# Kernel tuning notes

Measured on AMD Instinct MI355X. Metric: run time of the kernel, lower is better.

The kernel has to match this reference:

```python
import jax, jax.numpy as jnp
import numpy as np

B, S, D, T, H = 4, 2048, 1024, 5, 8


def setup_inputs() -> dict:
    key = jax.random.key(0)
    ks = jax.random.split(key, 12)
    sc = 0.02  # small init scale for weights so attention logits stay sane
    return {
        "x": jax.random.normal(ks[0], (B, S, D), jnp.float32),
        "time_steps": jax.random.randint(ks[1], (B, S), 0, T),
        "gamma": jnp.ones((T, D), jnp.float32),
        "beta": jax.random.normal(ks[2], (T, D), jnp.float32) * sc,
        "decay": jnp.ones((T,), jnp.float32),
        "shift_W": jax.random.normal(ks[3], (D, D), jnp.float32) * sc,
        "shift_b": jax.random.normal(ks[4], (D,), jnp.float32) * sc,
        "in_proj_W": jax.random.normal(ks[5], (3 * D, D), jnp.float32) * sc,
        "in_proj_b": jax.random.normal(ks[6], (3 * D,), jnp.float32) * sc,
        "out_proj_W": jax.random.normal(ks[7], (D, D), jnp.float32) * sc,
        "out_proj_b": jax.random.normal(ks[8], (D,), jnp.float32) * sc,
    }


def reference(x, time_steps, gamma, beta, decay, shift_W, shift_b,
              in_proj_W, in_proj_b, out_proj_W, out_proj_b):
    eps = 1e-5
    T_ = gamma.shape[0]
    b_, s_, d_ = x.shape
    hd = d_ // H

    # --- per-token indexed LayerNorm + decay (vectorized gather of norm params) ---
    idx = jnp.clip(time_steps, 0, T_ - 1)              # safe gather index [B,S]
    mu = jnp.mean(x, axis=-1, keepdims=True)
    var = jnp.mean(jnp.square(x - mu), axis=-1, keepdims=True)
    xn = (x - mu) * jax.lax.rsqrt(var + eps)           # [B,S,D]
    normed = (xn * gamma[idx] + beta[idx]) * decay[idx][..., None]
    x = jnp.where((time_steps < T_)[..., None], normed, x)

    # --- residual temporal shift (Linear) ---
    x = x + x @ shift_W.T + shift_b

    # --- torch-style MultiheadAttention(x, x, x), batch_first ---
    qkv = x @ in_proj_W.T + in_proj_b                  # [B,S,3D]
    q, k, v = jnp.split(qkv, 3, axis=-1)
    q = q.reshape(b_, s_, H, hd)
    k = k.reshape(b_, s_, H, hd)
    v = v.reshape(b_, s_, H, hd)
    scale = 1.0 / jnp.sqrt(jnp.asarray(hd, x.dtype))
    scores = jnp.einsum('bqhd,bkhd->bhqk', q, k) * scale   # [B,H,S,S]
    attn = jax.nn.softmax(scores, axis=-1)
    ctx = jnp.einsum('bhqk,bkhd->bqhd', attn, v).reshape(b_, s_, d_)
    attended = ctx @ out_proj_W.T + out_proj_b
    return x + attended
```

## Files before the change

### kernel.cpp

```cpp
#include <hip/hip_runtime.h>
#include <math.h>

#define B_ 4
#define S_ 2048
#define D_ 1024
#define T_ 5
#define H_ 8
#define HD_ 128
#define M_ (B_*S_)

typedef __bf16 bf16x8 __attribute__((ext_vector_type(8)));
typedef float  f32x4  __attribute__((ext_vector_type(4)));

__device__ __forceinline__ float bf2f(unsigned short u) {
    union { unsigned int i; float f; } c; c.i = ((unsigned int)u) << 16; return c.f;
}
__device__ __forceinline__ unsigned short f2bf(float f) {
    union { float f; unsigned int i; } c; c.f = f;
    unsigned int u = c.i;
    u += 0x7fffu + ((u >> 16) & 1u);
    return (unsigned short)(u >> 16);
}

__device__ __forceinline__ void gll16(const void* g, void* l) {
    __builtin_amdgcn_global_load_lds(
        (const __attribute__((address_space(1))) void*)g,
        (__attribute__((address_space(3))) void*)l, 16, 0, 0);
}

__global__ __launch_bounds__(256) void f2bf3_kernel(
    const float* __restrict__ s0,
    const float* __restrict__ s1,
    const float* __restrict__ s2,
    unsigned short* __restrict__ dst)
{
    int i = (blockIdx.x * 256 + threadIdx.x) * 4;
    const float* src;
    int local;
    if (i < D_ * D_)              { src = s0; local = i; }
    else if (i < 4 * D_ * D_)     { src = s1; local = i - D_ * D_; }
    else                          { src = s2; local = i - 4 * D_ * D_; }
    float4 v = *(const float4*)(src + local);
    ushort4 o;
    o.x = f2bf(v.x); o.y = f2bf(v.y); o.z = f2bf(v.z); o.w = f2bf(v.w);
    *(ushort4*)(dst + i) = o;
}

__global__ __launch_bounds__(256) void ln_kernel(
    const float* __restrict__ x, const int* __restrict__ ts,
    const float* __restrict__ gamma, const float* __restrict__ beta,
    const float* __restrict__ decay, unsigned short* __restrict__ out)
{
    int row = blockIdx.x;
    int tid = threadIdx.x;
    float4 v = ((const float4*)(x + (size_t)row * D_))[tid];
    float s  = v.x + v.y + v.z + v.w;
    float s2 = v.x*v.x + v.y*v.y + v.z*v.z + v.w*v.w;
    #pragma unroll
    for (int off = 32; off; off >>= 1) {
        s  += __shfl_down(s,  off);
        s2 += __shfl_down(s2, off);
    }
    __shared__ float ps[4], ps2[4];
    if ((tid & 63) == 0) { ps[tid >> 6] = s; ps2[tid >> 6] = s2; }
    __syncthreads();
    float tot  = ps[0]  + ps[1]  + ps[2]  + ps[3];
    float tot2 = ps2[0] + ps2[1] + ps2[2] + ps2[3];
    float mu   = tot  * (1.0f / D_);
    float var  = tot2 * (1.0f / D_) - mu * mu;
    float rstd = rsqrtf(var + 1e-5f);

    int t  = ts[row];
    int tc = min(max(t, 0), T_ - 1);
    float4 g = ((const float4*)(gamma + (size_t)tc * D_))[tid];
    float4 b = ((const float4*)(beta  + (size_t)tc * D_))[tid];
    float dec = decay[tc];

    float4 o;
    o.x = ((v.x - mu) * rstd * g.x + b.x) * dec;
    o.y = ((v.y - mu) * rstd * g.y + b.y) * dec;
    o.z = ((v.z - mu) * rstd * g.z + b.z) * dec;
    o.w = ((v.w - mu) * rstd * g.w + b.w) * dec;
    if (t >= T_) o = v;
    ushort4 ob;
    ob.x = f2bf(o.x); ob.y = f2bf(o.y); ob.z = f2bf(o.z); ob.w = f2bf(o.w);
    ((ushort4*)(out + (size_t)row * D_))[tid] = ob;
}

__global__ __launch_bounds__(256) void gemm_mfma(
    const unsigned short* __restrict__ A,
    const unsigned short* __restrict__ Wt,
    const float* __restrict__ bias,
    const float* __restrict__ ResF,
    const unsigned short* __restrict__ ResB,
    float* __restrict__ Cf,
    unsigned short* __restrict__ Cb,
    int M, int N, int K, int lda)
{
    __shared__ __align__(16) unsigned short SMEM[128 * 132];
    int tid  = threadIdx.x;
    int w    = tid >> 6, lane = tid & 63;
    int lm   = lane & 15, quad = lane >> 4;
    int wm   = w & 1,  wn   = w >> 1;

    int nwgx  = gridDim.x;
    int lin   = blockIdx.y * nwgx + blockIdx.x;
    int chunk = (nwgx * gridDim.y) >> 3;
    int swz   = (lin & 7) * chunk + (lin >> 3);
    int bx    = swz % nwgx, by = swz / nwgx;

    int i0 = by * 128, j0 = bx * 128;

    f32x4 acc[4][4];
    #pragma unroll
    for (int mt = 0; mt < 4; ++mt)
        #pragma unroll
        for (int nt = 0; nt < 4; ++nt)
            acc[mt][nt] = (f32x4){0.f, 0.f, 0.f, 0.f};

    int c0 = w * 128 + lane;
    int r0 = c0 >> 2,   k80 = (c0 & 3) * 8;
    int c1 = c0 + 64;
    int r1 = c1 >> 2,   k81 = (c1 & 3) * 8;

#define GEMM_STAGE(buf, ktt)                                                           \
    gll16(A  + (size_t)(i0 + r0) * lda + (ktt) + k80, SMEM + (buf)*4096 + (w*128+0 )*8);\
    gll16(A  + (size_t)(i0 + r1) * lda + (ktt) + k81, SMEM + (buf)*4096 + (w*128+64)*8);\
    gll16(Wt + (size_t)(j0 + r0) * K   + (ktt) + k80, SMEM + 8192 + (buf)*4096 + (w*128+0 )*8);\
    gll16(Wt + (size_t)(j0 + r1) * K   + (ktt) + k81, SMEM + 8192 + (buf)*4096 + (w*128+64)*8);

    GEMM_STAGE(0, 0)

    int cur = 0;
    for (int kt = 0; kt < K; kt += 32) {
        __syncthreads();
        if (kt + 32 < K) { GEMM_STAGE(cur ^ 1, kt + 32) }

        const unsigned short* Asc = SMEM + cur * 4096;
        const unsigned short* Bsc = SMEM + 8192 + cur * 4096;
        bf16x8 af[4], bfr[4];
        #pragma unroll
        for (int mt = 0; mt < 4; ++mt)
            af[mt] = *(const bf16x8*)&Asc[(wm * 64 + mt * 16 + lm) * 32 + quad * 8];
        #pragma unroll
        for (int nt = 0; nt < 4; ++nt)
            bfr[nt] = *(const bf16x8*)&Bsc[(wn * 64 + nt * 16 + lm) * 32 + quad * 8];
        #pragma unroll
        for (int mt = 0; mt < 4; ++mt)
            #pragma unroll
            for (int nt = 0; nt < 4; ++nt)
                acc[mt][nt] = __builtin_amdgcn_mfma_f32_16x16x32_bf16(
                    af[mt], bfr[nt], acc[mt][nt], 0, 0, 0);
        cur ^= 1;
    }
#undef GEMM_STAGE

    if (Cb != nullptr && Cf == nullptr) {
        __syncthreads();
        #pragma unroll
        for (int nt = 0; nt < 4; ++nt) {
            int lj = wn * 64 + nt * 16 + lm;
            float bj = bias[j0 + lj];
            #pragma unroll
            for (int mt = 0; mt < 4; ++mt) {
                #pragma unroll
                for (int r = 0; r < 4; ++r) {
                    int li = wm * 64 + mt * 16 + quad * 4 + r;
                    float v = acc[mt][nt][r] + bj;
                    if (ResB) v += bf2f(ResB[(size_t)(i0 + li) * N + j0 + lj]);
                    SMEM[li * 132 + lj] = f2bf(v);
                }
            }
        }
        __syncthreads();
        #pragma unroll
        for (int c = 0; c < 8; ++c) {
            int ch  = tid + 256 * c;
            int row = ch >> 4, col = (ch & 15) * 8;
            const unsigned short* srcp = &SMEM[row * 132 + col];
            uint2 q0 = *(const uint2*)(srcp);
            uint2 q1 = *(const uint2*)(srcp + 4);
            uint4 q; q.x = q0.x; q.y = q0.y; q.z = q1.x; q.w = q1.y;
            *(uint4*)(Cb + (size_t)(i0 + row) * N + j0 + col) = q;
        }
        return;
    }

    #pragma unroll
    for (int nt = 0; nt < 4; ++nt) {
        int j = j0 + wn * 64 + nt * 16 + lm;
        float bj = bias[j];
        #pragma unroll
        for (int mt = 0; mt < 4; ++mt) {
            #pragma unroll
            for (int r = 0; r < 4; ++r) {
                int i = i0 + wm * 64 + mt * 16 + quad * 4 + r;
                size_t off = (size_t)i * N + j;
                float v = acc[mt][nt][r] + bj;
                if (ResF) v += ResF[off];
                else if (ResB) v += bf2f(ResB[off]);
                if (Cf) Cf[off] = v;
                if (Cb) Cb[off] = f2bf(v);
            }
        }
    }
}

__global__ __launch_bounds__(256) void transpose_v(
    const unsigned short* __restrict__ qkv, unsigned short* __restrict__ vt)
{
    __shared__ unsigned short Ts[64][72];
    int t = threadIdx.x;
    int s0 = blockIdx.x * 64, c0 = blockIdx.y * 64, b = blockIdx.z;
    int r  = t >> 2, cg = (t & 3) * 16;
    const unsigned short* src =
        qkv + (size_t)(b * S_ + s0 + r) * (3 * D_) + 2 * D_ + c0 + cg;
    *(bf16x8*)&Ts[r][cg]     = *(const bf16x8*)(src);
    *(bf16x8*)&Ts[r][cg + 8] = *(const bf16x8*)(src + 8);
    __syncthreads();
    int dd = t >> 2, sg = (t & 3) * 16;
    unsigned short tmp[16];
    #pragma unroll
    for (int j = 0; j < 16; ++j) tmp[j] = Ts[sg + j][dd];
    unsigned short* dst = vt + ((size_t)b * D_ + c0 + dd) * S_ + s0 + sg;
    *(bf16x8*)dst       = *(bf16x8*)&tmp[0];
    *(bf16x8*)(dst + 8) = *(bf16x8*)&tmp[8];
}

__global__ __launch_bounds__(256, 2) void flash_mfma(
    const unsigned short* __restrict__ qkv,
    const unsigned short* __restrict__ vt,
    unsigned short* __restrict__ ctx)
{
    __shared__ __align__(16) unsigned short Ks [2][64 * 128];
    __shared__ __align__(16) unsigned short Vts[2][128 * 64];
    __shared__ __align__(16) unsigned short Ps [4][32 * 64];

    int tid  = threadIdx.x;
    int w    = tid >> 6, lane = tid & 63;
    int lm   = lane & 15, quad = lane >> 4;

    int lin0 = blockIdx.x + (blockIdx.y << 4) + (blockIdx.z << 7);
    int nl   = (lin0 & 7) * 64 + (lin0 >> 3);
    int qt   = nl & 15, h = (nl >> 4) & 7, b = nl >> 7;

    const int rs = 3 * D_;
    const float scale = 0.08838834764831844f;
    size_t qbase  = (size_t)b * S_ * rs + (size_t)h * HD_;
    size_t kbase  = qbase + D_;
    size_t vtbase = ((size_t)b * H_ + h) * (size_t)HD_ * S_;
    int q0 = qt * 128 + w * 32;

    int krow0 = w * 4 + (lane >> 4);
    int kcolE = ((((lane & 15) * 16) ^ ((krow0 & 7) << 4)) >> 1);
    int vrow0 = w * 8 + (lane >> 3);
    int vcolE = ((((lane & 7)  * 16) ^ ((vrow0 & 7) << 4)) >> 1);

    const int rxor = (lm & 7) << 4;

    #pragma unroll
    for (int i = 0; i < 4; ++i) {
        gll16(qkv + kbase + (size_t)(krow0 + 16 * i) * rs + kcolE,
              &Ks[0][i * 2048 + w * 512]);
        gll16(vt  + vtbase + (size_t)(vrow0 + 32 * i) * S_ + vcolE,
              &Vts[0][i * 2048 + w * 512]);
    }

    bf16x8 qf[2][4];
    #pragma unroll
    for (int mt = 0; mt < 2; ++mt)
        #pragma unroll
        for (int kc = 0; kc < 4; ++kc) {
            bf16x8 raw = *(const bf16x8*)(
                qkv + qbase + (size_t)(q0 + mt * 16 + lm) * rs + kc * 32 + quad * 8);
            bf16x8 sc;
            #pragma unroll
            for (int j = 0; j < 8; ++j)
                sc[j] = (__bf16)((float)raw[j] * scale);
            qf[mt][kc] = sc;
        }

    f32x4 oacc[2][8];
    #pragma unroll
    for (int mt = 0; mt < 2; ++mt)
        #pragma unroll
        for (int n = 0; n < 8; ++n)
            oacc[mt][n] = (f32x4){0.f, 0.f, 0.f, 0.f};
    float lst[2][4];
    #pragma unroll
    for (int mt = 0; mt < 2; ++mt)
        #pragma unroll
        for (int r = 0; r < 4; ++r) lst[mt][r] = 0.f;

    int cur = 0;
    for (int kt = 0; kt < S_ / 64; ++kt) {
        __syncthreads();

        if (kt + 1 < S_ / 64) {
            int k0n = (kt + 1) * 64, nb = cur ^ 1;
            #pragma unroll
            for (int i = 0; i < 4; ++i) {
                gll16(qkv + kbase + (size_t)(k0n + krow0 + 16 * i) * rs + kcolE,
                      &Ks[nb][i * 2048 + w * 512]);
                gll16(vt  + vtbase + (size_t)(vrow0 + 32 * i) * S_ + k0n + vcolE,
                      &Vts[nb][i * 2048 + w * 512]);
            }
        }

        const char* Kb = (const char*)&Ks[cur][0];
        const char* Vb = (const char*)&Vts[cur][0];

        f32x4 sacc[2][4];
        #pragma unroll
        for (int mt = 0; mt < 2; ++mt)
            #pragma unroll
            for (int n = 0; n < 4; ++n)
                sacc[mt][n] = (f32x4){0.f, 0.f, 0.f, 0.f};
        __builtin_amdgcn_s_setprio(1);
        #pragma unroll
        for (int n = 0; n < 4; ++n) {
            bf16x8 bk[4];
            #pragma unroll
            for (int kc = 0; kc < 4; ++kc)
                bk[kc] = *(const bf16x8*)(Kb + (n * 16 + lm) * 256 +
                                          ((kc * 64 + quad * 16) ^ rxor));
            #pragma unroll
            for (int mt = 0; mt < 2; ++mt)
                #pragma unroll
                for (int kc = 0; kc < 4; ++kc)
                    sacc[mt][n] = __builtin_amdgcn_mfma_f32_16x16x32_bf16(
                        qf[mt][kc], bk[kc], sacc[mt][n], 0, 0, 0);
        }
        __builtin_amdgcn_s_setprio(0);

        char* Pw = (char*)&Ps[w][0];
        #pragma unroll
        for (int mt = 0; mt < 2; ++mt) {
            #pragma unroll
            for (int r = 0; r < 4; ++r) {
                float p0 = __expf(sacc[mt][0][r]);
                float p1 = __expf(sacc[mt][1][r]);
                float p2 = __expf(sacc[mt][2][r]);
                float p3 = __expf(sacc[mt][3][r]);
                lst[mt][r] += (p0 + p1) + (p2 + p3);
                int row = mt * 16 + quad * 4 + r;
                int wx  = (row & 7) << 4;
                char* rowp = Pw + row * 128;
                *(unsigned short*)(rowp + (( 0 + lm * 2) ^ wx)) = f2bf(p0);
                *(unsigned short*)(rowp + ((32 + lm * 2) ^ wx)) = f2bf(p1);
                *(unsigned short*)(rowp + ((64 + lm * 2) ^ wx)) = f2bf(p2);
                *(unsigned short*)(rowp + ((96 + lm * 2) ^ wx)) = f2bf(p3);
            }
        }

        bf16x8 pa[2][2];
        #pragma unroll
        for (int mt = 0; mt < 2; ++mt)
            #pragma unroll
            for (int kc = 0; kc < 2; ++kc)
                pa[mt][kc] = *(const bf16x8*)(Pw + (mt * 16 + lm) * 128 +
                                              ((kc * 64 + quad * 16) ^ rxor));
        __builtin_amdgcn_s_setprio(1);
        #pragma unroll
        for (int n = 0; n < 8; ++n) {
            bf16x8 bv0 = *(const bf16x8*)(Vb + (n * 16 + lm) * 128 +
                                          (( 0 + quad * 16) ^ rxor));
            bf16x8 bv1 = *(const bf16x8*)(Vb + (n * 16 + lm) * 128 +
                                          ((64 + quad * 16) ^ rxor));
            #pragma unroll
            for (int mt = 0; mt < 2; ++mt) {
                oacc[mt][n] = __builtin_amdgcn_mfma_f32_16x16x32_bf16(
                    pa[mt][0], bv0, oacc[mt][n], 0, 0, 0);
                oacc[mt][n] = __builtin_amdgcn_mfma_f32_16x16x32_bf16(
                    pa[mt][1], bv1, oacc[mt][n], 0, 0, 0);
            }
        }
        __builtin_amdgcn_s_setprio(0);
        cur ^= 1;
    }

    float linv[2][4];
    #pragma unroll
    for (int mt = 0; mt < 2; ++mt)
        #pragma unroll
        for (int r = 0; r < 4; ++r) {
            float l = lst[mt][r];
            l += __shfl_xor(l, 1);
            l += __shfl_xor(l, 2);
            l += __shfl_xor(l, 4);
            l += __shfl_xor(l, 8);
            linv[mt][r] = 1.0f / l;
        }
    size_t rowbase = (size_t)b * S_ + (size_t)qt * 128 + w * 32;
    #pragma unroll
    for (int mt = 0; mt < 2; ++mt)
        #pragma unroll
        for (int r = 0; r < 4; ++r) {
            size_t row = rowbase + mt * 16 + quad * 4 + r;
            unsigned short* dst = ctx + row * (size_t)(3 * D_) + h * HD_ + lm;
            #pragma unroll
            for (int n = 0; n < 8; ++n)
                dst[n * 16] = f2bf(oacc[mt][n][r] * linv[mt][r]);
        }
}

extern "C" void kernel_launch(void* const* d_in, const int* in_sizes, int n_in,
                              void* d_out, int out_size, void* d_ws, size_t ws_size,
                              hipStream_t stream) {
    (void)in_sizes; (void)n_in; (void)out_size; (void)ws_size;
    const float* x          = (const float*)d_in[0];
    const int*   ts         = (const int*)  d_in[1];
    const float* gamma      = (const float*)d_in[2];
    const float* beta       = (const float*)d_in[3];
    const float* decay      = (const float*)d_in[4];
    const float* shift_W    = (const float*)d_in[5];
    const float* shift_b    = (const float*)d_in[6];
    const float* in_proj_W  = (const float*)d_in[7];
    const float* in_proj_b  = (const float*)d_in[8];
    const float* out_proj_W = (const float*)d_in[9];
    const float* out_proj_b = (const float*)d_in[10];
    float* out = (float*)d_out;

    unsigned short* p     = (unsigned short*)d_ws;
    unsigned short* xln_b = p;
    unsigned short* qkv_b = xln_b + (size_t)M_ * D_;
    unsigned short* xs_b  = qkv_b + (size_t)M_ * 3 * D_;
    unsigned short* wsh_b = xs_b  + (size_t)M_ * D_;
    unsigned short* wip_b = wsh_b + (size_t)D_ * D_;
    unsigned short* wop_b = wip_b + (size_t)3 * D_ * D_;
    unsigned short* vt_b  = xln_b;
    unsigned short* ctx_b = qkv_b + 2 * D_;

    f2bf3_kernel<<<5 * D_ * D_ / 1024, 256, 0, stream>>>(
        shift_W, in_proj_W, out_proj_W, wsh_b);

    ln_kernel<<<M_, 256, 0, stream>>>(x, ts, gamma, beta, decay, xln_b);

    gemm_mfma<<<dim3(D_ / 128, M_ / 128), 256, 0, stream>>>(
        xln_b, wsh_b, shift_b, nullptr, xln_b, nullptr, xs_b, M_, D_, D_, D_);

    gemm_mfma<<<dim3(3 * D_ / 128, M_ / 128), 256, 0, stream>>>(
        xs_b, wip_b, in_proj_b, nullptr, nullptr, nullptr, qkv_b, M_, 3 * D_, D_, D_);

    transpose_v<<<dim3(S_ / 64, D_ / 64, B_), 256, 0, stream>>>(qkv_b, vt_b);
    flash_mfma<<<dim3(S_ / 128, H_, B_), 256, 0, stream>>>(qkv_b, vt_b, ctx_b);

    gemm_mfma<<<dim3(D_ / 128, M_ / 128), 256, 0, stream>>>(
        ctx_b, wop_b, out_proj_b, nullptr, xs_b, out, nullptr, M_, D_, D_, 3 * D_);
}
```

Before: 357.4 us.

## Use 256x256-tile 512-thread GEMM for QKV projection; use native bf16 conversion in attention

Adds a new GEMM kernel with 256x256 output tiles, 8 waves, double-buffered LDS staging via global_load_lds, block-index swizzling for L2 locality, and a coalesced epilogue that goes through shared memory. It replaces the 128x128 GEMM for the in-projection to raise data reuse per loaded tile. Separately, the flash attention kernel switches its manual float-to-bf16 rounding to the compiler's native bf16 cast to cut conversion instructions. The larger tile uses more registers and LDS per block, which may lower occupancy. The grid of 12x32 blocks may also leave CUs unevenly loaded.

```diff
diff --git a/kernel.cpp b/kernel.cpp
--- a/kernel.cpp
+++ b/kernel.cpp
@@ -20,6 +20,10 @@
     unsigned int u = c.i;
     u += 0x7fffu + ((u >> 16) & 1u);
     return (unsigned short)(u >> 16);
+}
+__device__ __forceinline__ unsigned short bfc(float f) {
+    __bf16 h = (__bf16)f;
+    unsigned short u; __builtin_memcpy(&u, &h, 2); return u;
 }
 
 __device__ __forceinline__ void gll16(const void* g, void* l) {
@@ -206,6 +210,101 @@
     }
 }
 
+__global__ __launch_bounds__(512, 2) void gemm_mfma256(
+    const unsigned short* __restrict__ A,
+    const unsigned short* __restrict__ Wt,
+    const float* __restrict__ bias,
+    unsigned short* __restrict__ Cb,
+    int M, int N, int K)
+{
+    __shared__ __align__(16) unsigned short SMEM[128 * 272];
+    int tid  = threadIdx.x;
+    int w    = tid >> 6, lane = tid & 63;
+    int lm   = lane & 15, quad = lane >> 4;
+    int wm   = w & 1,  wn   = w >> 1;
+
+    int nwgx  = gridDim.x;
+    int lin   = blockIdx.y * nwgx + blockIdx.x;
+    int chunk = (nwgx * gridDim.y) >> 3;
+    int swz   = (lin & 7) * chunk + (lin >> 3);
+    int bx    = swz % nwgx, by = swz / nwgx;
+
+    int i0 = by * 256, j0 = bx * 256;
+
+    f32x4 acc[8][4];
+    #pragma unroll
+    for (int mt = 0; mt < 8; ++mt)
+        #pragma unroll
+        for (int nt = 0; nt < 4; ++nt)
+            acc[mt][nt] = (f32x4){0.f, 0.f, 0.f, 0.f};
+
+    int c0 = w * 64 + lane;
+    int r0 = c0 >> 2, k8 = (c0 & 3) * 8;
+
+#define STAGE256(buf, ktt)                                                             \
+    gll16(A  + (size_t)(i0 + r0      ) * K + (ktt) + k8, SMEM + (buf)*8192 + (w*64)*8);\
+    gll16(A  + (size_t)(i0 + r0 + 128) * K + (ktt) + k8, SMEM + (buf)*8192 + 4096 + (w*64)*8);\
+    gll16(Wt + (size_t)(j0 + r0      ) * K + (ktt) + k8, SMEM + 16384 + (buf)*8192 + (w*64)*8);\
+    gll16(Wt + (size_t)(j0 + r0 + 128) * K + (ktt) + k8, SMEM + 16384 + (buf)*8192 + 4096 + (w*64)*8);
+
+    STAGE256(0, 0)
+
+    int cur = 0;
+    for (int kt = 0; kt < K; kt += 32) {
+        __syncthreads();
+        if (kt + 32 < K) { STAGE256(cur ^ 1, kt + 32) }
+
+        const unsigned short* Asc = SMEM + cur * 8192;
+        const unsigned short* Bsc = SMEM + 16384 + cur * 8192;
+        bf16x8 af[8], bfr[4];
+        #pragma unroll
+        for (int mt = 0; mt < 8; ++mt)
+            af[mt] = *(const bf16x8*)&Asc[(wm * 128 + mt * 16 + lm) * 32 + quad * 8];
+        #pragma unroll
+        for (int nt = 0; nt < 4; ++nt)
+            bfr[nt] = *(const bf16x8*)&Bsc[(wn * 64 + nt * 16 + lm) * 32 + quad * 8];
+        #pragma unroll
+        for (int mt = 0; mt < 8; ++mt)
+            #pragma unroll
+            for (int nt = 0; nt < 4; ++nt)
+                acc[mt][nt] = __builtin_amdgcn_mfma_f32_16x16x32_bf16(
+                    af[mt], bfr[nt], acc[mt][nt], 0, 0, 0);
+        cur ^= 1;
+    }
+#undef STAGE256
+
+    #pragma unroll
+    for (int hb = 0; hb < 2; ++hb) {
+        __syncthreads();
+        if (wm == hb) {
+            #pragma unroll
+            for (int nt = 0; nt < 4; ++nt) {
+                int lj = wn * 64 + nt * 16 + lm;
+                float bj = bias[j0 + lj];
+                #pragma unroll
+                for (int mt = 0; mt < 8; ++mt) {
+                    #pragma unroll
+                    for (int r = 0; r < 4; ++r) {
+                        int li = mt * 16 + quad * 4 + r;
+                        SMEM[li * 272 + lj] = f2bf(acc[mt][nt][r] + bj);
+                    }
+                }
+            }
+        }
+        __syncthreads();
+        #pragma unroll
+        for (int c = 0; c < 8; ++c) {
+            int ch  = tid + 512 * c;
+            int row = ch >> 5, col = (ch & 31) * 8;
+            const unsigned short* srcp = &SMEM[row * 272 + col];
+            uint2 q0 = *(const uint2*)(srcp);
+            uint2 q1 = *(const uint2*)(srcp + 4);
+            uint4 q; q.x = q0.x; q.y = q0.y; q.z = q1.x; q.w = q1.y;
+            *(uint4*)(Cb + (size_t)(i0 + hb * 128 + row) * N + j0 + col) = q;
+        }
+    }
+}
+
 __global__ __launch_bounds__(256) void transpose_v(
     const unsigned short* __restrict__ qkv, unsigned short* __restrict__ vt)
 {
@@ -346,10 +445,10 @@
                 int row = mt * 16 + quad * 4 + r;
                 int wx  = (row & 7) << 4;
                 char* rowp = Pw + row * 128;
-                *(unsigned short*)(rowp + (( 0 + lm * 2) ^ wx)) = f2bf(p0);
-                *(unsigned short*)(rowp + ((32 + lm * 2) ^ wx)) = f2bf(p1);
-                *(unsigned short*)(rowp + ((64 + lm * 2) ^ wx)) = f2bf(p2);
-                *(unsigned short*)(rowp + ((96 + lm * 2) ^ wx)) = f2bf(p3);
+                *(unsigned short*)(rowp + (( 0 + lm * 2) ^ wx)) = bfc(p0);
+                *(unsigned short*)(rowp + ((32 + lm * 2) ^ wx)) = bfc(p1);
+                *(unsigned short*)(rowp + ((64 + lm * 2) ^ wx)) = bfc(p2);
+                *(unsigned short*)(rowp + ((96 + lm * 2) ^ wx)) = bfc(p3);
             }
         }
 
@@ -400,7 +499,7 @@
             unsigned short* dst = ctx + row * (size_t)(3 * D_) + h * HD_ + lm;
             #pragma unroll
             for (int n = 0; n < 8; ++n)
-                dst[n * 16] = f2bf(oacc[mt][n][r] * linv[mt][r]);
+                dst[n * 16] = bfc(oacc[mt][n][r] * linv[mt][r]);
         }
 }
 
@@ -439,8 +538,8 @@
     gemm_mfma<<<dim3(D_ / 128, M_ / 128), 256, 0, stream>>>(
         xln_b, wsh_b, shift_b, nullptr, xln_b, nullptr, xs_b, M_, D_, D_, D_);
 
-    gemm_mfma<<<dim3(3 * D_ / 128, M_ / 128), 256, 0, stream>>>(
-        xs_b, wip_b, in_proj_b, nullptr, nullptr, nullptr, qkv_b, M_, 3 * D_, D_, D_);
+    gemm_mfma256<<<dim3(3 * D_ / 256, M_ / 256), 512, 0, stream>>>(
+        xs_b, wip_b, in_proj_b, qkv_b, M_, 3 * D_, D_);
 
     transpose_v<<<dim3(S_ / 64, D_ / 64, B_), 256, 0, stream>>>(qkv_b, vt_b);
     flash_mfma<<<dim3(S_ / 128, H_, B_), 256, 0, stream>>>(qkv_b, vt_b, ctx_b);
```

Measured after the change: 342.2 us. 4.3% less time.
